# Performance work log

Measured on AMD Instinct MI355X. Metric: run time of the kernel, lower is better.

Reference implementation:

```python
import math
import jax, jax.numpy as jnp
import numpy as np

B, S, D = 4, 4096, 1024
H = 16
DH = D // H          # 64
INNER = H * DH       # 1024
EPS = 1e-6


def _layernorm(z, g, b):
    m = jnp.mean(z, axis=-1, keepdims=True)
    v = jnp.mean((z - m) ** 2, axis=-1, keepdims=True)
    return (z - m) * jax.lax.rsqrt(v + EPS) * g + b


def _pos_encoding(seq_len, d_model, dtype):
    pos = jnp.arange(seq_len, dtype=jnp.float32)[:, None]                    # [S,1]
    div = jnp.exp(jnp.arange(0, d_model, 2, dtype=jnp.float32)
                  * (-math.log(10000.0) / d_model))                          # [D/2]
    pe = jnp.zeros((seq_len, d_model), dtype=jnp.float32)
    pe = pe.at[:, 0::2].set(jnp.sin(pos * div))
    pe = pe.at[:, 1::2].set(jnp.cos(pos * div))
    return pe.astype(dtype)[None]                                            # [1,S,D]


def setup_inputs() -> dict:
    key = jax.random.key(0)
    ks = jax.random.split(key, 8)
    std = 0.02
    x = jax.random.normal(ks[0], (B, S, D), dtype=jnp.float32)
    inp = {
        "x": x,
        "ln1_g": jnp.ones((D,), jnp.float32),
        "ln1_b": jnp.zeros((D,), jnp.float32),
        "Wqkv": std * jax.random.normal(ks[1], (D, 3 * INNER), jnp.float32),
        "Wo": std * jax.random.normal(ks[2], (INNER, D), jnp.float32),
        "bo": jnp.zeros((D,), jnp.float32),
        "ln2_g": jnp.ones((D,), jnp.float32),
        "ln2_b": jnp.zeros((D,), jnp.float32),
        "W1": std * jax.random.normal(ks[3], (D, D), jnp.float32),
        "b1": jnp.zeros((D,), jnp.float32),
        "W2": std * jax.random.normal(ks[4], (D, D), jnp.float32),
        "b2": jnp.zeros((D,), jnp.float32),
    }
    return inp


def reference(x, ln1_g, ln1_b, Wqkv, Wo, bo, ln2_g, ln2_b, W1, b1, W2, b2):
    # --- ln_1 + positional encoding (dropout p=0) ---
    h = _layernorm(x, ln1_g, ln1_b)
    h = h + _pos_encoding(h.shape[1], h.shape[2], h.dtype)
    # --- linear self-attention (non-causal, efficient attention) ---
    qkv = h @ Wqkv                                                           # [B,S,3*INNER]
    q, k, v = jnp.split(qkv, 3, axis=-1)
    def heads(t):  # [B,S,INNER] -> [B,H,S,DH]
        return t.reshape(B, S, H, DH).transpose(0, 2, 1, 3)
    q, k, v = heads(q), heads(k), heads(v)
    q = jax.nn.softmax(q, axis=-1) * (DH ** -0.5)
    k = jax.nn.softmax(k, axis=-2)
    ctx = jnp.einsum("bhnd,bhne->bhde", k, v)                               # [B,H,DH,DH]
    attn_out = jnp.einsum("bhnd,bhde->bhne", q, ctx)                        # [B,H,S,DH]
    attn_out = attn_out.transpose(0, 2, 1, 3).reshape(B, S, INNER)
    attn_out = attn_out @ Wo + bo
    # --- residual, ln_2, MLP (Linear -> GELU -> Linear), residual ---
    x = x + attn_out
    y = _layernorm(x, ln2_g, ln2_b)
    y = jax.nn.gelu(y @ W1 + b1, approximate=False) @ W2 + b2
    return x + y
```

## Files before the change

### kernel.cpp

```cpp
#include <hip/hip_runtime.h>
#include <hip/hip_bf16.h>
#include <math.h>

#define B_   4
#define S_   4096
#define D_   1024
#define H_   16
#define DH_  64
#define BS_  (B_ * S_)
#define N3_  3072

using bf16 = __hip_bfloat16;
typedef __attribute__((ext_vector_type(8))) short bf16x8;
typedef __attribute__((ext_vector_type(4))) float f32x4;

#define GAS __attribute__((address_space(1)))
#define LAS __attribute__((address_space(3)))

__device__ __forceinline__ void gload_lds16(const bf16* g, bf16* l) {
  __builtin_amdgcn_global_load_lds((const GAS void*)g, (LAS void*)l, 16, 0, 0);
}

__device__ __forceinline__ float bf2f(short u) {
  unsigned int x = ((unsigned int)(unsigned short)u) << 16;
  return __builtin_bit_cast(float, x);
}
__device__ __forceinline__ unsigned short f2bfu(float f) {
  bf16 t = __float2bfloat16(f);
  return *(unsigned short*)&t;
}

__global__ __launch_bounds__(256)
void transpose_cast4(const float* __restrict__ Wqkv, const float* __restrict__ Wo,
                     const float* __restrict__ W1, const float* __restrict__ W2,
                     bf16* __restrict__ wqkvt, bf16* __restrict__ wot,
                     bf16* __restrict__ w1t, bf16* __restrict__ w2t)
{
  __shared__ float tile[32][33];
  int gx = blockIdx.x;
  const float* W; bf16* Wt; int N, xo;
  if (gx < 96)        { W = Wqkv; Wt = wqkvt; N = N3_; xo = gx; }
  else if (gx < 128)  { W = Wo;   Wt = wot;   N = D_;  xo = gx - 96; }
  else if (gx < 160)  { W = W1;   Wt = w1t;   N = D_;  xo = gx - 128; }
  else                { W = W2;   Wt = w2t;   N = D_;  xo = gx - 160; }
  int n0 = xo * 32, k0 = blockIdx.y * 32;
  int tx = threadIdx.x & 31, ty = threadIdx.x >> 5;
#pragma unroll
  for (int j = 0; j < 32; j += 8)
    tile[ty + j][tx] = W[(size_t)(k0 + ty + j) * N + n0 + tx];
  __syncthreads();
#pragma unroll
  for (int j = 0; j < 32; j += 8)
    Wt[(size_t)(n0 + ty + j) * 1024 + k0 + tx] = __float2bfloat16(tile[tx][ty + j]);
}

template<bool PE, bool INBF16>
__global__ __launch_bounds__(256)
void ln_kernel(const float* __restrict__ Xf, const bf16* __restrict__ Xb,
               const float* __restrict__ G, const float* __restrict__ Bv,
               bf16* __restrict__ out)
{
  int row = blockIdx.x;
  int t = threadIdx.x;
  float4 v;
  if (INBF16) {
    ushort4 u = ((const ushort4*)Xb)[(size_t)row * (D_ / 4) + t];
    v.x = bf2f(u.x); v.y = bf2f(u.y); v.z = bf2f(u.z); v.w = bf2f(u.w);
  } else {
    v = ((const float4*)(Xf + (size_t)row * D_))[t];
  }
  float s  = v.x + v.y + v.z + v.w;
  float ss = v.x * v.x + v.y * v.y + v.z * v.z + v.w * v.w;
#pragma unroll
  for (int o = 32; o > 0; o >>= 1) { s += __shfl_xor(s, o); ss += __shfl_xor(ss, o); }
  __shared__ float red[8];
  int wid = t >> 6, lane = t & 63;
  if (lane == 0) { red[wid] = s; red[4 + wid] = ss; }
  __syncthreads();
  s  = red[0] + red[1] + red[2] + red[3];
  ss = red[4] + red[5] + red[6] + red[7];
  float mean = s * (1.0f / D_);
  float var  = ss * (1.0f / D_) - mean * mean;
  float rs   = rsqrtf(var + 1e-6f);
  int d0 = t * 4;
  const float4 g4 = ((const float4*)G)[t];
  const float4 b4 = ((const float4*)Bv)[t];
  float o0 = (v.x - mean) * rs * g4.x + b4.x;
  float o1 = (v.y - mean) * rs * g4.y + b4.y;
  float o2 = (v.z - mean) * rs * g4.z + b4.z;
  float o3 = (v.w - mean) * rs * g4.w + b4.w;
  if (PE) {
    const float C = -0.0089944730194f;
    float p = (float)(row & (S_ - 1));
    float sn, cs;
    __sincosf(p * __expf((float)d0 * C), &sn, &cs);        o0 += sn; o1 += cs;
    __sincosf(p * __expf((float)(d0 + 2) * C), &sn, &cs);  o2 += sn; o3 += cs;
  }
  ushort4 pk;
  pk.x = f2bfu(o0); pk.y = f2bfu(o1); pk.z = f2bfu(o2); pk.w = f2bfu(o3);
  ((ushort4*)out)[(size_t)row * (D_ / 4) + t] = pk;
}

enum { EPI_QKV = 0, EPI_BIAS_RES_BF16 = 1, EPI_BIAS_GELU_BF16 = 2, EPI_BIAS_RESB_F32 = 3 };

#define MFMA_ __builtin_amdgcn_mfma_f32_16x16x32_bf16

template<int EPI, bool AHM>
__global__ __launch_bounds__(512)
void gemm256(const bf16* __restrict__ A, const bf16* __restrict__ Bt,
             float* __restrict__ Cf, bf16* __restrict__ Cb,
             const float* __restrict__ bias, const float* __restrict__ resf,
             const bf16* __restrict__ resb,
             bf16* __restrict__ Ck, bf16* __restrict__ Cv,
             int M, int N, int K)
{
  extern __shared__ __align__(16) char smem[];
  bf16* lds = (bf16*)smem;

  const int t = threadIdx.x;
  const int wid = t >> 6, lane = t & 63;
  const int wr = wid >> 2, wc = wid & 3;
  const int bid = blockIdx.x;
  const int c = bid & 7;
  const int w = bid >> 3;
  const int sst = w >> 4;
  const int ii = w & 15;
  const int txg = sst >> 1, tyg = sst & 1;
  const int iy = ii & 3, ix = ii >> 2;
  const int ty = c * 8 + tyg * 4 + iy;
  const int tx = txg * 4 + ix;
  const int m0 = ty << 8, n0 = tx << 8;

  const bf16* Ab = AHM
      ? A + (((size_t)(m0 >> 12) * 16) * 4096 + (m0 & 4095)) * 64
      : A + (size_t)m0 * K;
  const bf16* Bb = Bt + (size_t)n0 * K;

  const int srow = t >> 2;
  const int scol = (((t & 3) ^ ((t >> 3) & 3)) * 8);
  const int NT = K >> 6;
  const int fr = lane & 15;
  const int fksw = (((lane >> 4) ^ ((lane >> 1) & 3)) * 8);

  f32x4 acc[8][4] = {};

  #define LDSHALF(b, mat, kh) (lds + (((((b) << 1) + (mat)) << 1) + (kh)) * 8192)

  #define STAGE(kt, mat, kh) do {                                              \
    bf16* _dst = LDSHALF((kt) & 1, (mat), (kh)) + t * 8;                       \
    const int _ktk = (kt) & (NT - 1);                                          \
    if ((mat) == 0 && AHM) {                                                   \
      const bf16* _sb = Ab + (size_t)_ktk * 262144 + (size_t)srow * 64         \
                        + (kh) * 32 + scol;                                    \
      gload_lds16(_sb, _dst);                                                  \
      gload_lds16(_sb + 8192, _dst + 4096);                                    \
    } else {                                                                   \
      const bf16* _sb = ((mat) == 0 ? Ab : Bb) + (size_t)srow * K              \
                        + (_ktk << 6) + (kh) * 32 + scol;                      \
      gload_lds16(_sb, _dst);                                                  \
      gload_lds16(_sb + (size_t)128 * K, _dst + 4096);                         \
    }                                                                          \
  } while (0)

  STAGE(0, 0, 0); STAGE(0, 1, 0);
  STAGE(0, 0, 1); STAGE(0, 1, 1);
  asm volatile("s_waitcnt vmcnt(4)" ::: "memory");
  __builtin_amdgcn_s_barrier();

#pragma unroll 2
  for (int kt = 0; kt < NT; ++kt) {
    const int cur = kt & 1;
    const bf16* hA0 = LDSHALF(cur, 0, 0);
    const bf16* hB0 = LDSHALF(cur, 1, 0);
    const bf16* hA1 = LDSHALF(cur, 0, 1);
    const bf16* hB1 = LDSHALF(cur, 1, 1);
    bf16x8 a[8], b0, b1, b2, b3;

#pragma unroll
    for (int mi = 0; mi < 8; ++mi)
      a[mi] = *(const bf16x8*)&hA0[(wr * 128 + mi * 16 + fr) * 32 + fksw];
    b0 = *(const bf16x8*)&hB0[(wc * 64 +  0 + fr) * 32 + fksw];
    b1 = *(const bf16x8*)&hB0[(wc * 64 + 16 + fr) * 32 + fksw];
    STAGE(kt + 1, 0, 0);
    __builtin_amdgcn_s_barrier();
    __builtin_amdgcn_s_setprio(1);
#pragma unroll
    for (int mi = 0; mi < 8; ++mi) {
      acc[mi][0] = MFMA_(a[mi], b0, acc[mi][0], 0, 0, 0);
      acc[mi][1] = MFMA_(a[mi], b1, acc[mi][1], 0, 0, 0);
    }
    __builtin_amdgcn_s_setprio(0);
    __builtin_amdgcn_s_barrier();

    b2 = *(const bf16x8*)&hB0[(wc * 64 + 32 + fr) * 32 + fksw];
    b3 = *(const bf16x8*)&hB0[(wc * 64 + 48 + fr) * 32 + fksw];
    STAGE(kt + 1, 1, 0);
    __builtin_amdgcn_s_barrier();
    __builtin_amdgcn_s_setprio(1);
#pragma unroll
    for (int mi = 0; mi < 8; ++mi) {
      acc[mi][2] = MFMA_(a[mi], b2, acc[mi][2], 0, 0, 0);
      acc[mi][3] = MFMA_(a[mi], b3, acc[mi][3], 0, 0, 0);
    }
    __builtin_amdgcn_s_setprio(0);
    asm volatile("s_waitcnt vmcnt(4)" ::: "memory");
    __builtin_amdgcn_s_barrier();

#pragma unroll
    for (int mi = 0; mi < 8; ++mi)
      a[mi] = *(const bf16x8*)&hA1[(wr * 128 + mi * 16 + fr) * 32 + fksw];
    b0 = *(const bf16x8*)&hB1[(wc * 64 +  0 + fr) * 32 + fksw];
    b1 = *(const bf16x8*)&hB1[(wc * 64 + 16 + fr) * 32 + fksw];
    STAGE(kt + 1, 0, 1);
    __builtin_amdgcn_s_barrier();
    __builtin_amdgcn_s_setprio(1);
#pragma unroll
    for (int mi = 0; mi < 8; ++mi) {
      acc[mi][0] = MFMA_(a[mi], b0, acc[mi][0], 0, 0, 0);
      acc[mi][1] = MFMA_(a[mi], b1, acc[mi][1], 0, 0, 0);
    }
    __builtin_amdgcn_s_setprio(0);
    __builtin_amdgcn_s_barrier();

    b2 = *(const bf16x8*)&hB1[(wc * 64 + 32 + fr) * 32 + fksw];
    b3 = *(const bf16x8*)&hB1[(wc * 64 + 48 + fr) * 32 + fksw];
    STAGE(kt + 1, 1, 1);
    __builtin_amdgcn_s_barrier();
    __builtin_amdgcn_s_setprio(1);
#pragma unroll
    for (int mi = 0; mi < 8; ++mi) {
      acc[mi][2] = MFMA_(a[mi], b2, acc[mi][2], 0, 0, 0);
      acc[mi][3] = MFMA_(a[mi], b3, acc[mi][3], 0, 0, 0);
    }
    __builtin_amdgcn_s_setprio(0);
    asm volatile("s_waitcnt vmcnt(4)" ::: "memory");
    __builtin_amdgcn_s_barrier();
  }
  asm volatile("s_waitcnt vmcnt(0)" ::: "memory");

  const int brow = m0 >> 12;
  const int mrow = m0 & 4095;
#pragma unroll
  for (int mi = 0; mi < 8; ++mi) {
    int rowb = m0 + wr * 128 + mi * 16 + (lane >> 4) * 4;
#pragma unroll
    for (int ni = 0; ni < 4; ++ni) {
      int col = n0 + wc * 64 + ni * 16 + fr;
      if (EPI == EPI_QKV) {
        int qsel = col >> 10;
        int hh = (col >> 6) & 15;
        int dd = col & 63;
        int sloc = mrow + wr * 128 + mi * 16 + (lane >> 4) * 4;
        if (qsel == 0) {
          unsigned short* qp = (unsigned short*)Cb +
            (((size_t)(brow * 16 + hh) * 4096 + sloc) * 64 + dd);
#pragma unroll
          for (int j = 0; j < 4; ++j)
            qp[(size_t)j * 64] = f2bfu(acc[mi][ni][j]);
        } else {
          unsigned short* kp = (unsigned short*)(qsel == 1 ? Ck : Cv) +
            (((size_t)(brow * 16 + hh) * 64 + dd) * 4096 + sloc);
          ushort4 pk;
          pk.x = f2bfu(acc[mi][ni][0]); pk.y = f2bfu(acc[mi][ni][1]);
          pk.z = f2bfu(acc[mi][ni][2]); pk.w = f2bfu(acc[mi][ni][3]);
          *(ushort4*)kp = pk;
        }
      } else {
#pragma unroll
        for (int j = 0; j < 4; ++j) {
          int row = rowb + j;
          float v = acc[mi][ni][j];
          if (EPI == EPI_BIAS_RES_BF16) {
            Cb[(size_t)row * N + col] =
              __float2bfloat16(v + bias[col] + resf[(size_t)row * N + col]);
          } else if (EPI == EPI_BIAS_GELU_BF16) {
            float u = v + bias[col];
            u = 0.5f * u * (1.0f + erff(u * 0.70710678118654752f));
            Cb[(size_t)row * N + col] = __float2bfloat16(u);
          } else {
            Cf[(size_t)row * N + col] =
              v + bias[col] + bf2f(*(const short*)&resb[(size_t)row * N + col]);
          }
        }
      }
    }
  }
  #undef STAGE
  #undef LDSHALF
}

__global__ __launch_bounds__(256)
void ctx_kernel(const bf16* __restrict__ kT, const bf16* __restrict__ vT,
                bf16* __restrict__ ctxT)
{
  int bh = blockIdx.x;
  int t = threadIdx.x, lane = t & 63, wid = t >> 6;
  __shared__ float partials[4][4096];
  __shared__ float rden[64];
  __shared__ float denp[256];

  {
    int d = t >> 2, part = t & 3;
    const unsigned short* kp = (const unsigned short*)kT +
      ((size_t)bh * 64 + d) * 4096 + part * 1024;
    float s = 0.f;
    for (int i = 0; i < 128; ++i) {
      bf16x8 k8 = *(const bf16x8*)(kp + i * 8);
#pragma unroll
      for (int j = 0; j < 8; ++j) s += __expf(bf2f(k8[j]));
    }
    denp[t] = s;
  }
  __syncthreads();
  if (t < 64) rden[t] = 1.0f / (denp[t*4] + denp[t*4+1] + denp[t*4+2] + denp[t*4+3]);

  const int fr = lane & 15, g = lane >> 4;
  f32x4 acc[4][4] = {};
  const unsigned short* kb = (const unsigned short*)kT + (size_t)bh * 64 * 4096;
  const unsigned short* vb = (const unsigned short*)vT + (size_t)bh * 64 * 4096;
  for (int i = 0; i < 32; ++i) {
    int kofs = wid * 1024 + i * 32 + g * 8;
    bf16x8 av[4], bv[4];
#pragma unroll
    for (int mi = 0; mi < 4; ++mi) {
      bf16x8 kr = *(const bf16x8*)(kb + (size_t)(mi * 16 + fr) * 4096 + kofs);
      bf16x8 ae;
#pragma unroll
      for (int j = 0; j < 8; ++j) ae[j] = (short)f2bfu(__expf(bf2f(kr[j])));
      av[mi] = ae;
      bv[mi] = *(const bf16x8*)(vb + (size_t)(mi * 16 + fr) * 4096 + kofs);
    }
#pragma unroll
    for (int mi = 0; mi < 4; ++mi)
#pragma unroll
      for (int ni = 0; ni < 4; ++ni)
        acc[mi][ni] = MFMA_(av[mi], bv[ni], acc[mi][ni], 0, 0, 0);
  }
#pragma unroll
  for (int mi = 0; mi < 4; ++mi)
#pragma unroll
    for (int ni = 0; ni < 4; ++ni)
      *(f32x4*)&partials[wid][(mi * 4 + ni) * 256 + lane * 4] = acc[mi][ni];
  __syncthreads();

  int lane2 = t & 63, fg = t >> 6;
  int fr2 = lane2 & 15, g2 = lane2 >> 4;
#pragma unroll
  for (int ff = 0; ff < 4; ++ff) {
    int f = fg * 4 + ff;
    int mi = f >> 2, ni = f & 3;
    f32x4 s = {};
#pragma unroll
    for (int ww = 0; ww < 4; ++ww)
      s += *(const f32x4*)&partials[ww][f * 256 + lane2 * 4];
    int e = ni * 16 + fr2;
    int d0 = mi * 16 + g2 * 4;
    ushort4 pk;
    pk.x = f2bfu(s[0] * rden[d0 + 0]);
    pk.y = f2bfu(s[1] * rden[d0 + 1]);
    pk.z = f2bfu(s[2] * rden[d0 + 2]);
    pk.w = f2bfu(s[3] * rden[d0 + 3]);
    *(ushort4*)((unsigned short*)ctxT + ((size_t)bh * 64 + e) * 64 + d0) = pk;
  }
}

__global__ __launch_bounds__(256)
void attn_kernel(const bf16* __restrict__ qhm, const bf16* __restrict__ ctxT,
                 bf16* __restrict__ attn)
{
  int blk = blockIdx.x;
  int chunk = blk & 15, bh = blk >> 4;
  int t = threadIdx.x, lane = t & 63, wid = t >> 6;
  __shared__ bf16 P[256 * 64];
  __shared__ bf16 CT[64 * 64];

  {
    const unsigned short* cg = (const unsigned short*)ctxT + (size_t)bh * 4096;
#pragma unroll
    for (int r = 0; r < 2; ++r) {
      int idx = r * 256 + t;
      int e = idx >> 3, b = idx & 7;
      bf16x8 v = *(const bf16x8*)(cg + idx * 8);
      *(bf16x8*)&CT[e * 64 + ((b ^ (e & 7)) * 8)] = v;
    }
  }
  {
    int s = chunk * 256 + t;
    const unsigned short* qp = (const unsigned short*)qhm + ((size_t)bh * 4096 + s) * 64;
    float p[64];
#pragma unroll
    for (int j = 0; j < 8; ++j) {
      bf16x8 q8 = *(const bf16x8*)(qp + j * 8);
#pragma unroll
      for (int i = 0; i < 8; ++i) p[j * 8 + i] = bf2f(q8[i]);
    }
    float mx = p[0];
#pragma unroll
    for (int d = 1; d < 64; ++d) mx = fmaxf(mx, p[d]);
    float sum = 0.f;
#pragma unroll
    for (int d = 0; d < 64; ++d) { p[d] = __expf(p[d] - mx); sum += p[d]; }
    float f = 0.125f / sum;
    bf16* pb = &P[(t >> 6) * 4096 + (t & 63) * 64];
#pragma unroll
    for (int b = 0; b < 8; ++b) {
      bf16x8 pk;
#pragma unroll
      for (int i = 0; i < 8; ++i) pk[i] = (short)f2bfu(p[b * 8 + i] * f);
      *(bf16x8*)&pb[((b ^ (t & 7)) * 8)] = pk;
    }
  }
  __syncthreads();

  const int fr = lane & 15, g = lane >> 4;
  f32x4 acc[4][4] = {};
  const bf16* Pw = &P[wid * 4096];
#pragma unroll
  for (int ks = 0; ks < 2; ++ks) {
    bf16x8 av[4], bv[4];
#pragma unroll
    for (int mi = 0; mi < 4; ++mi) {
      int r = mi * 16 + fr;
      av[mi] = *(const bf16x8*)&Pw[r * 64 + (((ks * 4 + g) ^ (r & 7)) * 8)];
    }
#pragma unroll
    for (int ni = 0; ni < 4; ++ni) {
      int e = ni * 16 + fr;
      bv[ni] = *(const bf16x8*)&CT[e * 64 + (((ks * 4 + g) ^ (e & 7)) * 8)];
    }
#pragma unroll
    for (int mi = 0; mi < 4; ++mi)
#pragma unroll
      for (int ni = 0; ni < 4; ++ni)
        acc[mi][ni] = MFMA_(av[mi], bv[ni], acc[mi][ni], 0, 0, 0);
  }
  unsigned short* ob = (unsigned short*)attn +
      ((size_t)bh * 4096 + chunk * 256 + wid * 64) * 64;
#pragma unroll
  for (int mi = 0; mi < 4; ++mi)
#pragma unroll
    for (int ni = 0; ni < 4; ++ni) {
      int e = ni * 16 + fr;
#pragma unroll
      for (int j = 0; j < 4; ++j) {
        int r = mi * 16 + g * 4 + j;
        ob[(size_t)r * 64 + e] = f2bfu(acc[mi][ni][j]);
      }
    }
}

#define OFF_WQKVT  ((size_t)0)
#define OFF_WOT    ((size_t)6291456)
#define OFF_W1T    ((size_t)8388608)
#define OFF_W2T    ((size_t)10485760)
#define OFF_CTXT   ((size_t)12582912)
#define OFF_ATTN   ((size_t)33554432)
#define OFF_H      OFF_ATTN
#define OFF_QHM    ((size_t)67108864)
#define OFF_KT     ((size_t)100663296)
#define OFF_VT     ((size_t)134217728)
#define OFF_Z      OFF_QHM
#define OFF_X2B    OFF_KT
#define OFF_Y      OFF_VT

extern "C" void kernel_launch(void* const* d_in, const int* in_sizes, int n_in,
                              void* d_out, int out_size, void* d_ws, size_t ws_size,
                              hipStream_t stream)
{
  const float* x     = (const float*)d_in[0];
  const float* ln1_g = (const float*)d_in[1];
  const float* ln1_b = (const float*)d_in[2];
  const float* Wqkv  = (const float*)d_in[3];
  const float* Wo    = (const float*)d_in[4];
  const float* bo    = (const float*)d_in[5];
  const float* ln2_g = (const float*)d_in[6];
  const float* ln2_b = (const float*)d_in[7];
  const float* W1    = (const float*)d_in[8];
  const float* b1    = (const float*)d_in[9];
  const float* W2    = (const float*)d_in[10];
  const float* b2    = (const float*)d_in[11];
  float* out = (float*)d_out;
  char* ws = (char*)d_ws;

  bf16*  h     = (bf16*)(ws + OFF_H);
  bf16*  attn  = (bf16*)(ws + OFF_ATTN);
  bf16*  qhm   = (bf16*)(ws + OFF_QHM);
  bf16*  kT    = (bf16*)(ws + OFF_KT);
  bf16*  vT    = (bf16*)(ws + OFF_VT);
  bf16*  ctxT  = (bf16*)(ws + OFF_CTXT);
  bf16*  x2b   = (bf16*)(ws + OFF_X2B);
  bf16*  y     = (bf16*)(ws + OFF_Y);
  bf16*  z     = (bf16*)(ws + OFF_Z);
  bf16*  wqkvt = (bf16*)(ws + OFF_WQKVT);
  bf16*  wot   = (bf16*)(ws + OFF_WOT);
  bf16*  w1t   = (bf16*)(ws + OFF_W1T);
  bf16*  w2t   = (bf16*)(ws + OFF_W2T);

  const size_t GEMM_LDS = 131072;

  transpose_cast4<<<dim3(192, 32), 256, 0, stream>>>(Wqkv, Wo, W1, W2,
                                                     wqkvt, wot, w1t, w2t);

  ln_kernel<true, false><<<BS_, 256, 0, stream>>>(x, nullptr, ln1_g, ln1_b, h);

  gemm256<EPI_QKV, false><<<(N3_ / 256) * (BS_ / 256), 512, GEMM_LDS, stream>>>(
      h, wqkvt, nullptr, qhm, nullptr, nullptr, nullptr, kT, vT, BS_, N3_, D_);

  ctx_kernel<<<64, 256, 0, stream>>>(kT, vT, ctxT);

  attn_kernel<<<1024, 256, 0, stream>>>(qhm, ctxT, attn);

  gemm256<EPI_BIAS_RES_BF16, true><<<(D_ / 256) * (BS_ / 256), 512, GEMM_LDS, stream>>>(
      attn, wot, nullptr, x2b, bo, x, nullptr, nullptr, nullptr, BS_, D_, D_);

  ln_kernel<false, true><<<BS_, 256, 0, stream>>>(nullptr, x2b, ln2_g, ln2_b, y);

  gemm256<EPI_BIAS_GELU_BF16, false><<<(D_ / 256) * (BS_ / 256), 512, GEMM_LDS, stream>>>(
      y, w1t, nullptr, z, b1, nullptr, nullptr, nullptr, nullptr, BS_, D_, D_);

  gemm256<EPI_BIAS_RESB_F32, false><<<(D_ / 256) * (BS_ / 256), 512, GEMM_LDS, stream>>>(
      z, w2t, out, nullptr, b2, nullptr, x2b, nullptr, nullptr, BS_, D_, D_);
}
```

Baseline: 383.0 us.

## Split context reduction over sequence chunks into partial and merge kernels

The single ctx kernel used only 64 blocks, one per batch-head, which leaves most compute units idle. It is now split into ctx_partial, which runs 512 blocks over 8 sequence chunks, and ctx_merge, which sums the partial context and denominator results. The softmax denominator is now accumulated from the same exp values used for the MFMA operands, so the separate pass over K is gone. The cost is an extra kernel launch and a round trip of fp32 partials through global memory.

```diff
diff --git a/kernel.cpp b/kernel.cpp
--- a/kernel.cpp
+++ b/kernel.cpp
@@ -290,43 +290,37 @@
 }
 
 __global__ __launch_bounds__(256)
-void ctx_kernel(const bf16* __restrict__ kT, const bf16* __restrict__ vT,
-                bf16* __restrict__ ctxT)
-{
-  int bh = blockIdx.x;
+void ctx_partial(const bf16* __restrict__ kT, const bf16* __restrict__ vT,
+                 float* __restrict__ pctx, float* __restrict__ pden)
+{
+  int blk = blockIdx.x;
+  int kc = blk & 7, bh = blk >> 3;
   int t = threadIdx.x, lane = t & 63, wid = t >> 6;
-  __shared__ float partials[4][4096];
-  __shared__ float rden[64];
-  __shared__ float denp[256];
-
-  {
-    int d = t >> 2, part = t & 3;
-    const unsigned short* kp = (const unsigned short*)kT +
-      ((size_t)bh * 64 + d) * 4096 + part * 1024;
-    float s = 0.f;
-    for (int i = 0; i < 128; ++i) {
-      bf16x8 k8 = *(const bf16x8*)(kp + i * 8);
-#pragma unroll
-      for (int j = 0; j < 8; ++j) s += __expf(bf2f(k8[j]));
-    }
-    denp[t] = s;
-  }
-  __syncthreads();
-  if (t < 64) rden[t] = 1.0f / (denp[t*4] + denp[t*4+1] + denp[t*4+2] + denp[t*4+3]);
-
   const int fr = lane & 15, g = lane >> 4;
+  __shared__ float part[4][4096];
+  __shared__ float dpart[4][64];
+
   f32x4 acc[4][4] = {};
+  float dsum[4] = {0.f, 0.f, 0.f, 0.f};
   const unsigned short* kb = (const unsigned short*)kT + (size_t)bh * 64 * 4096;
   const unsigned short* vb = (const unsigned short*)vT + (size_t)bh * 64 * 4096;
-  for (int i = 0; i < 32; ++i) {
-    int kofs = wid * 1024 + i * 32 + g * 8;
+  const int kbase = kc * 512 + wid * 128;
+#pragma unroll
+  for (int i = 0; i < 4; ++i) {
+    int kofs = kbase + i * 32 + g * 8;
     bf16x8 av[4], bv[4];
 #pragma unroll
     for (int mi = 0; mi < 4; ++mi) {
       bf16x8 kr = *(const bf16x8*)(kb + (size_t)(mi * 16 + fr) * 4096 + kofs);
       bf16x8 ae;
-#pragma unroll
-      for (int j = 0; j < 8; ++j) ae[j] = (short)f2bfu(__expf(bf2f(kr[j])));
+      float es = 0.f;
+#pragma unroll
+      for (int j = 0; j < 8; ++j) {
+        float e = __expf(bf2f(kr[j]));
+        es += e;
+        ae[j] = (short)f2bfu(e);
+      }
+      dsum[mi] += es;
       av[mi] = ae;
       bv[mi] = *(const bf16x8*)(vb + (size_t)(mi * 16 + fr) * 4096 + kofs);
     }
@@ -337,13 +331,47 @@
         acc[mi][ni] = MFMA_(av[mi], bv[ni], acc[mi][ni], 0, 0, 0);
   }
 #pragma unroll
+  for (int mi = 0; mi < 4; ++mi) {
+    dsum[mi] += __shfl_xor(dsum[mi], 16);
+    dsum[mi] += __shfl_xor(dsum[mi], 32);
+  }
+#pragma unroll
   for (int mi = 0; mi < 4; ++mi)
 #pragma unroll
     for (int ni = 0; ni < 4; ++ni)
-      *(f32x4*)&partials[wid][(mi * 4 + ni) * 256 + lane * 4] = acc[mi][ni];
+      *(f32x4*)&part[wid][(mi * 4 + ni) * 256 + lane * 4] = acc[mi][ni];
+  if (g == 0) {
+#pragma unroll
+    for (int mi = 0; mi < 4; ++mi) dpart[wid][mi * 16 + fr] = dsum[mi];
+  }
   __syncthreads();
-
   int lane2 = t & 63, fg = t >> 6;
+#pragma unroll
+  for (int ff = 0; ff < 4; ++ff) {
+    int f = fg * 4 + ff;
+    f32x4 s = {};
+#pragma unroll
+    for (int ww = 0; ww < 4; ++ww)
+      s += *(const f32x4*)&part[ww][f * 256 + lane2 * 4];
+    *(f32x4*)&pctx[((size_t)blk * 16 + f) * 256 + lane2 * 4] = s;
+  }
+  if (t < 64)
+    pden[blk * 64 + t] = dpart[0][t] + dpart[1][t] + dpart[2][t] + dpart[3][t];
+}
+
+__global__ __launch_bounds__(256)
+void ctx_merge(const float* __restrict__ pctx, const float* __restrict__ pden,
+               bf16* __restrict__ ctxT)
+{
+  int bh = blockIdx.x;
+  int t = threadIdx.x, lane2 = t & 63, fg = t >> 6;
+  __shared__ float rden[64];
+  if (t < 64) {
+    float s = 0.f;
+    for (int kc = 0; kc < 8; ++kc) s += pden[(bh * 8 + kc) * 64 + t];
+    rden[t] = 1.0f / s;
+  }
+  __syncthreads();
   int fr2 = lane2 & 15, g2 = lane2 >> 4;
 #pragma unroll
   for (int ff = 0; ff < 4; ++ff) {
@@ -351,8 +379,8 @@
     int mi = f >> 2, ni = f & 3;
     f32x4 s = {};
 #pragma unroll
-    for (int ww = 0; ww < 4; ++ww)
-      s += *(const f32x4*)&partials[ww][f * 256 + lane2 * 4];
+    for (int kc = 0; kc < 8; ++kc)
+      s += *(const f32x4*)&pctx[(((size_t)(bh * 8 + kc)) * 16 + f) * 256 + lane2 * 4];
     int e = ni * 16 + fr2;
     int d0 = mi * 16 + g2 * 4;
     ushort4 pk;
@@ -454,6 +482,8 @@
 #define OFF_W1T    ((size_t)8388608)
 #define OFF_W2T    ((size_t)10485760)
 #define OFF_CTXT   ((size_t)12582912)
+#define OFF_PCTX   ((size_t)13631488)
+#define OFF_PDEN   ((size_t)22020096)
 #define OFF_ATTN   ((size_t)33554432)
 #define OFF_H      OFF_ATTN
 #define OFF_QHM    ((size_t)67108864)
@@ -488,6 +518,8 @@
   bf16*  kT    = (bf16*)(ws + OFF_KT);
   bf16*  vT    = (bf16*)(ws + OFF_VT);
   bf16*  ctxT  = (bf16*)(ws + OFF_CTXT);
+  float* pctx  = (float*)(ws + OFF_PCTX);
+  float* pden  = (float*)(ws + OFF_PDEN);
   bf16*  x2b   = (bf16*)(ws + OFF_X2B);
   bf16*  y     = (bf16*)(ws + OFF_Y);
   bf16*  z     = (bf16*)(ws + OFF_Z);
@@ -506,7 +538,8 @@
   gemm256<EPI_QKV, false><<<(N3_ / 256) * (BS_ / 256), 512, GEMM_LDS, stream>>>(
       h, wqkvt, nullptr, qhm, nullptr, nullptr, nullptr, kT, vT, BS_, N3_, D_);
 
-  ctx_kernel<<<64, 256, 0, stream>>>(kT, vT, ctxT);
+  ctx_partial<<<512, 256, 0, stream>>>(kT, vT, pctx, pden);
+  ctx_merge<<<64, 256, 0, stream>>>(pctx, pden, ctxT);
 
   attn_kernel<<<1024, 256, 0, stream>>>(qhm, ctxT, attn);
 
```

Result: faster. 353.6 us (-7.7%).
